# Performance work log

Measured on AMD Instinct MI355X. Metric: run time of the kernel, lower is better.

Reference implementation:

```python
import jax, jax.numpy as jnp
import numpy as np

B, T, V = 64, 8192, 50257


def setup_inputs() -> dict:
    key = jax.random.key(0)
    k1, k2, k3, k4 = jax.random.split(key, 4)
    ids = jax.random.randint(k1, (B, T), 1, V, dtype=jnp.int32)
    # give each row a random real length in [T//2, T], rest padding (pad_token_id=0)
    lens = jax.random.randint(k4, (B,), T // 2, T + 1, dtype=jnp.int32)
    pos = jnp.arange(T, dtype=jnp.int32)[None, :]
    input_ids = jnp.where(pos < lens[:, None], ids, 0)
    is_punct = jax.random.uniform(k2, (V,)) < 0.05
    is_abbreviation = jax.random.uniform(k3, (V,)) < 0.01
    return {
        "input_ids": input_ids,
        "is_punct": is_punct,
        "is_abbreviation": is_abbreviation,
        "max_phrase_len": 32,
        "pad_token_id": 0,
    }


def reference(input_ids, is_punct, is_abbreviation, max_phrase_len, pad_token_id):
    Bb, Tt = input_ids.shape
    # ---- compute_is_end ----
    punct_at_t = is_punct[input_ids]                               # (B,T)
    prev_ids = jnp.concatenate(
        [jnp.zeros((Bb, 1), input_ids.dtype), input_ids[:, :-1]], axis=1)
    prev_is_abbr = is_abbreviation[prev_ids].at[:, 0].set(False)
    is_real = input_ids != pad_token_id                            # (B,T)
    pos = jnp.arange(Tt, dtype=jnp.int32)
    pos_bt = jnp.broadcast_to(pos[None, :], (Bb, Tt))
    last_real = jnp.max(jnp.where(is_real, pos_bt, -1), axis=1)    # (B,)
    is_end0 = punct_at_t & ~prev_is_abbr & is_real                 # pre-scan boundaries

    def step(last_boundary, xs):
        e_t, t = xs
        forced = (t - last_boundary) >= max_phrase_len
        fire = (e_t | (last_real == t) | forced) & (t <= last_real)
        last_boundary = jnp.where(fire, t, last_boundary)
        return last_boundary, fire

    _, fires = jax.lax.scan(
        step, jnp.full((Bb,), -1, jnp.int32),
        (is_end0.T, jnp.arange(Tt, dtype=jnp.int32)))
    is_end = fires.T                                               # (B,T) bool

    # ---- pack_phrases_from_is_end (P padded to T upper bound) ----
    ie = is_end.astype(jnp.int32)
    phrase_id = jnp.concatenate(
        [jnp.zeros((Bb, 1), jnp.int32), jnp.cumsum(ie[:, :-1], axis=1)], axis=1)
    P = Tt
    rows = jnp.arange(Bb, dtype=jnp.int32)[:, None]
    first_pos = jnp.full((Bb, P), Tt, jnp.int32).at[rows, phrase_id].min(pos_bt)
    slot = pos_bt - jnp.take_along_axis(first_pos, phrase_id, axis=1)  # (B,T)
    in_range = (slot < max_phrase_len) & (slot >= 0) & is_real
    # route invalid entries to a dummy slot (index max_phrase_len), slice it off
    safe_slot = jnp.where(in_range, slot, max_phrase_len)
    mask_pad = jnp.zeros((Bb, P, max_phrase_len + 1), bool)
    mask_pad = mask_pad.at[rows, phrase_id, safe_slot].set(in_range)
    phrase_mask = mask_pad[:, :, :max_phrase_len]
    tok_pad = jnp.zeros((Bb, P, max_phrase_len + 1), jnp.int32)
    tok_pad = tok_pad.at[rows, phrase_id, safe_slot].set(jnp.where(in_range, pos_bt, 0))
    phrase_token_idx = tok_pad[:, :, :max_phrase_len]
    phrase_end_pos = jnp.full((Bb, P), -1, jnp.int32).at[rows, phrase_id].max(
        jnp.where(in_range, pos_bt, -1))
    return phrase_mask, phrase_token_idx, phrase_end_pos
```

## Files before the change

kernel.cpp:

```cpp
#include <hip/hip_runtime.h>
#include <stdint.h>

#define BB 64
#define TT 8192

#define WS_PAIR   4096

__device__ __forceinline__ unsigned long long bitsBelow(int e) {
    return (e >= 64) ? ~0ULL : ((1ULL << e) - 1ULL);
}

__device__ __forceinline__ bool lut(const void* tbl, int flag, int idx) {
    if (flag == 2) return ((const float*)tbl)[idx]   != 0.0f;
    if (flag == 1) return ((const uint8_t*)tbl)[idx] != 0;
    return ((const int*)tbl)[idx] != 0;
}

__global__ __launch_bounds__(256) void natural_kernel(
        const int* __restrict__ ids,
        const void* __restrict__ punct,
        const void* __restrict__ abbr,
        ulonglong2* __restrict__ pairW) {
    __shared__ int sFlag;
    if (threadIdx.x == 0) sFlag = 0;
    __syncthreads();
    {
        const uint32_t* w = (const uint32_t*)punct;
        bool byteGT1 = false, wordGT1 = false;
#pragma unroll
        for (int j = 0; j < 4; ++j) {
            uint32_t x = w[threadIdx.x * 4 + j];
            byteGT1 |= (x & 0xFEFEFEFEu) != 0u;
            wordGT1 |= (x > 1u);
        }
        int local = (byteGT1 ? 2 : 0) | (wordGT1 ? 1 : 0);
        if (local) atomicOr(&sFlag, local);
    }
    __syncthreads();
    int fl = sFlag;
    int flag = (fl & 2) ? 2 : (fl & 1);

    int g = blockIdx.x * 256 + threadIdx.x;
    int t = g & (TT - 1);
    int id = ids[g];
    bool real = (id != 0);
    bool isLR = real && ((t == TT - 1) || (ids[g + 1] == 0));
    bool e = false;
    if (real) {
        bool pu = lut(punct, flag, id);
        if (pu) {
            bool pa = (t > 0) ? lut(abbr, flag, ids[g - 1]) : false;
            e = !pa;
        }
    }
    bool natural = real && (e || isLR);
    unsigned long long nb = __ballot(natural);
    unsigned long long rb = __ballot(real);
    if ((threadIdx.x & 63) == 0) {
        pairW[g >> 6] = make_ulonglong2(nb, rb);
    }
}

__global__ __launch_bounds__(1024) void fill_kernel(
        const ulonglong2* __restrict__ pairW,
        int* __restrict__ out) {
    __shared__ int sFires[TT];
    __shared__ int sNf;

    int b     = blockIdx.x >> 3;
    int slice = blockIdx.x & 7;
    int tid   = threadIdx.x;
    int wave  = tid >> 6, lane = tid & 63;

    if (wave == 0) {
        ulonglong2 pA = pairW[b * 128 + lane];
        ulonglong2 pB = pairW[b * 128 + 64 + lane];
        unsigned long long nA = pA.x, rA = pA.y;
        unsigned long long nB = pB.x, rB = pB.y;
        int lnA = nA ? lane * 64 + 63 - __clzll(nA) : -1;
        int lnB = nB ? (lane + 64) * 64 + 63 - __clzll(nB) : -1;
        int sA = lnA;
        for (int d = 1; d < 64; d <<= 1) { int v = __shfl_up(sA, d); if (lane >= d) sA = max(sA, v); }
        int exA = __shfl_up(sA, 1); if (lane == 0) exA = -1;
        int totA = __shfl(sA, 63);
        int sB = lnB;
        for (int d = 1; d < 64; d <<= 1) { int v = __shfl_up(sB, d); if (lane >= d) sB = max(sB, v); }
        int exB = __shfl_up(sB, 1); if (lane == 0) exB = -1;
        exB = max(exB, totA);

        auto fireWord = [&](unsigned long long nw, unsigned long long rw,
                            int widx, int carry) -> unsigned long long {
            long long base = (long long)widx * 64;
            unsigned long long fire = 0, rem = nw;
            long long cur = carry;
            while (true) {
                int nxt = rem ? (__ffsll(rem) - 1) : 64;
                int r = (int)(((cur - base) % 32 + 32) % 32);
                unsigned long long pat = (1ULL << r) | (1ULL << (r + 32));
                int s = (int)(cur - base + 1); if (s < 0) s = 0;
                fire |= pat & bitsBelow(nxt) & ~bitsBelow(s);
                if (!rem) break;
                fire |= 1ULL << nxt;
                cur = base + nxt;
                rem &= rem - 1;
            }
            return fire & rw;
        };
        unsigned long long fA = fireWord(nA, rA, lane, exA);
        unsigned long long fB = fireWord(nB, rB, lane + 64, exB);
        int pcA = __popcll(fA), pcB = __popcll(fB);
        int iA = pcA;
        for (int d = 1; d < 64; d <<= 1) { int v = __shfl_up(iA, d); if (lane >= d) iA += v; }
        int baseA = iA - pcA;
        int totPA = __shfl(iA, 63);
        int iB = pcB;
        for (int d = 1; d < 64; d <<= 1) { int v = __shfl_up(iB, d); if (lane >= d) iB += v; }
        int baseB = totPA + iB - pcB;
        int total = totPA + __shfl(iB, 63);
        unsigned long long f = fA; int idx = baseA;
        while (f) { int t = __ffsll(f) - 1; sFires[idx++] = lane * 64 + t; f &= f - 1; }
        f = fB; idx = baseB;
        while (f) { int t = __ffsll(f) - 1; sFires[idx++] = (lane + 64) * 64 + t; f &= f - 1; }
        if (lane == 0) sNf = total;
    }
    __syncthreads();

    int nf = sNf;
    const long long MOFF = (long long)BB * TT * 32;
    int pbase = slice * 1024;
#pragma unroll
    for (int i = 0; i < 8; ++i) {
        int task = i * 1024 + tid;
        int q  = task & 7;
        int lp = task >> 3;
        int gp = pbase + lp;
        int4 mv, tv;
        if (gp < nf) {
            int end   = sFires[gp];
            int start = (gp > 0) ? (sFires[gp - 1] + 1) : 0;
            int len   = end - start + 1;
            int s0 = q * 4;
            int* mp = (int*)&mv;
            int* tp = (int*)&tv;
#pragma unroll
            for (int j = 0; j < 4; ++j) {
                int s = s0 + j;
                bool m = s < len;
                mp[j] = m ? 1 : 0;
                tp[j] = m ? (start + s) : 0;
            }
        } else {
            mv = make_int4(0, 0, 0, 0);
            tv = mv;
        }
        long long bp = (long long)b * TT + gp;
        *(int4*)(out + bp * 32 + q * 4)        = mv;
        *(int4*)(out + MOFF + bp * 32 + q * 4) = tv;
    }
    {
        int gp = pbase + tid;
        out[2 * MOFF + (long long)b * TT + gp] = (gp < nf) ? sFires[gp] : -1;
    }
}

extern "C" void kernel_launch(void* const* d_in, const int* in_sizes, int n_in,
                              void* d_out, int out_size, void* d_ws, size_t ws_size,
                              hipStream_t stream) {
    const int*  ids   = (const int*)d_in[0];
    const void* punct = d_in[1];
    const void* abbr  = d_in[2];
    char* ws = (char*)d_ws;
    ulonglong2* pairW = (ulonglong2*)(ws + WS_PAIR);
    int* out = (int*)d_out;

    natural_kernel<<<(BB * TT) / 256, 256, 0, stream>>>(ids, punct, abbr, pairW);
    fill_kernel   <<<BB * 8, 1024, 0, stream>>>(pairW, out);
}
```

Measured before the change: 32.06 us.

## Pack lookup tables into bitmaps and fuse boundary detection into fill kernel

A small first kernel now compresses the punctuation and abbreviation tables into bitmaps. The boundary-detection work moves into the fill kernel: each block reads its row's ids, looks them up in the bitmaps, and builds the natural and real bit words in shared memory. This removes the global pairW round trip, and the lookups hit a small, cache-friendly bitmap instead of the full table. The trade-off is that the row's ids are now read by all 8 slice blocks, and the lookup work is repeated 8 times per row.

Measured after the change: 37.09 us. +15.7%, slower.

```diff
diff --git a/kernel.cpp b/kernel.cpp
--- a/kernel.cpp
+++ b/kernel.cpp
@@ -3,8 +3,11 @@
 
 #define BB 64
 #define TT 8192
-
-#define WS_PAIR   4096
+#define VV 50257
+
+#define NBMW 1571
+#define WS_BMP   4096
+#define WS_BMA   (4096 + 6400)
 
 __device__ __forceinline__ unsigned long long bitsBelow(int e) {
     return (e >= 64) ? ~0ULL : ((1ULL << e) - 1ULL);
@@ -16,11 +19,9 @@
     return ((const int*)tbl)[idx] != 0;
 }
 
-__global__ __launch_bounds__(256) void natural_kernel(
-        const int* __restrict__ ids,
-        const void* __restrict__ punct,
-        const void* __restrict__ abbr,
-        ulonglong2* __restrict__ pairW) {
+__global__ __launch_bounds__(256) void bitmap_kernel(
+        const void* __restrict__ punct, const void* __restrict__ abbr,
+        uint32_t* __restrict__ bmP, uint32_t* __restrict__ bmA) {
     __shared__ int sFlag;
     if (threadIdx.x == 0) sFlag = 0;
     __syncthreads();
@@ -40,30 +41,26 @@
     int fl = sFlag;
     int flag = (fl & 2) ? 2 : (fl & 1);
 
-    int g = blockIdx.x * 256 + threadIdx.x;
-    int t = g & (TT - 1);
-    int id = ids[g];
-    bool real = (id != 0);
-    bool isLR = real && ((t == TT - 1) || (ids[g + 1] == 0));
-    bool e = false;
-    if (real) {
-        bool pu = lut(punct, flag, id);
-        if (pu) {
-            bool pa = (t > 0) ? lut(abbr, flag, ids[g - 1]) : false;
-            e = !pa;
-        }
-    }
-    bool natural = real && (e || isLR);
-    unsigned long long nb = __ballot(natural);
-    unsigned long long rb = __ballot(real);
+    int nb = (int)gridDim.x >> 1;
+    int isAbbr = blockIdx.x >= nb;
+    int j = isAbbr ? (blockIdx.x - nb) : blockIdx.x;
+    const void* tbl = isAbbr ? abbr : punct;
+    uint32_t* out   = isAbbr ? bmA : bmP;
+    int i = j * 256 + threadIdx.x;
+    bool bit = (i < VV) ? lut(tbl, flag, i) : false;
+    unsigned long long bal = __ballot(bit);
     if ((threadIdx.x & 63) == 0) {
-        pairW[g >> 6] = make_ulonglong2(nb, rb);
-    }
-}
-
-__global__ __launch_bounds__(1024) void fill_kernel(
-        const ulonglong2* __restrict__ pairW,
+        *(unsigned long long*)&out[i >> 5] = bal;
+    }
+}
+
+__global__ __launch_bounds__(1024) void mono_kernel(
+        const int* __restrict__ ids,
+        const uint32_t* __restrict__ bmP,
+        const uint32_t* __restrict__ bmA,
         int* __restrict__ out) {
+    __shared__ unsigned long long sNat[128], sReal[128];
+    __shared__ uint8_t sBN[1024], sBR[1024];
     __shared__ int sFires[TT];
     __shared__ int sNf;
 
@@ -72,11 +69,42 @@
     int tid   = threadIdx.x;
     int wave  = tid >> 6, lane = tid & 63;
 
+    const int* rowIds = ids + b * TT;
+    int base = tid * 8;
+    int4 va = *(const int4*)(rowIds + base);
+    int4 vc = *(const int4*)(rowIds + base + 4);
+    int id[9];
+    id[0]=va.x; id[1]=va.y; id[2]=va.z; id[3]=va.w;
+    id[4]=vc.x; id[5]=vc.y; id[6]=vc.z; id[7]=vc.w;
+    id[8] = (tid < 1023) ? rowIds[base + 8] : 0;
+    int prev = (tid > 0) ? rowIds[base - 1] : 0;
+    uint32_t nbits = 0, rbits = 0;
+#pragma unroll
+    for (int j = 0; j < 8; ++j) {
+        int idj = id[j];
+        bool real = (idj != 0);
+        bool isLR = real && ((base + j == TT - 1) || (id[j + 1] == 0));
+        bool e = false;
+        if (real && ((bmP[idj >> 5] >> (idj & 31)) & 1u)) {
+            int pid = j ? id[j - 1] : prev;
+            e = (base + j == 0) ? true : !((bmA[pid >> 5] >> (pid & 31)) & 1u);
+        }
+        bool nat = real && (e || isLR);
+        nbits |= (uint32_t)nat  << j;
+        rbits |= (uint32_t)real << j;
+    }
+    sBN[tid] = (uint8_t)nbits;
+    sBR[tid] = (uint8_t)rbits;
+    __syncthreads();
+    if (tid < 128) {
+        sNat[tid]  = *(const unsigned long long*)&sBN[tid * 8];
+        sReal[tid] = *(const unsigned long long*)&sBR[tid * 8];
+    }
+    __syncthreads();
+
     if (wave == 0) {
-        ulonglong2 pA = pairW[b * 128 + lane];
-        ulonglong2 pB = pairW[b * 128 + 64 + lane];
-        unsigned long long nA = pA.x, rA = pA.y;
-        unsigned long long nB = pB.x, rB = pB.y;
+        unsigned long long nA = sNat[lane],  nB = sNat[lane + 64];
+        unsigned long long rA = sReal[lane], rB = sReal[lane + 64];
         int lnA = nA ? lane * 64 + 63 - __clzll(nA) : -1;
         int lnB = nB ? (lane + 64) * 64 + 63 - __clzll(nB) : -1;
         int sA = lnA;
@@ -90,18 +118,18 @@
 
         auto fireWord = [&](unsigned long long nw, unsigned long long rw,
                             int widx, int carry) -> unsigned long long {
-            long long base = (long long)widx * 64;
+            long long wbase = (long long)widx * 64;
             unsigned long long fire = 0, rem = nw;
             long long cur = carry;
             while (true) {
                 int nxt = rem ? (__ffsll(rem) - 1) : 64;
-                int r = (int)(((cur - base) % 32 + 32) % 32);
+                int r = (int)(((cur - wbase) % 32 + 32) % 32);
                 unsigned long long pat = (1ULL << r) | (1ULL << (r + 32));
-                int s = (int)(cur - base + 1); if (s < 0) s = 0;
+                int s = (int)(cur - wbase + 1); if (s < 0) s = 0;
                 fire |= pat & bitsBelow(nxt) & ~bitsBelow(s);
                 if (!rem) break;
                 fire |= 1ULL << nxt;
-                cur = base + nxt;
+                cur = wbase + nxt;
                 rem &= rem - 1;
             }
             return fire & rw;
@@ -170,9 +198,11 @@
     const void* punct = d_in[1];
     const void* abbr  = d_in[2];
     char* ws = (char*)d_ws;
-    ulonglong2* pairW = (ulonglong2*)(ws + WS_PAIR);
+    uint32_t* bmP = (uint32_t*)(ws + WS_BMP);
+    uint32_t* bmA = (uint32_t*)(ws + WS_BMA);
     int* out = (int*)d_out;
 
-    natural_kernel<<<(BB * TT) / 256, 256, 0, stream>>>(ids, punct, abbr, pairW);
-    fill_kernel   <<<BB * 8, 1024, 0, stream>>>(pairW, out);
-}
+    const int nb = (VV + 255) / 256;
+    bitmap_kernel<<<2 * nb, 256, 0, stream>>>(punct, abbr, bmP, bmA);
+    mono_kernel  <<<BB * 8, 1024, 0, stream>>>(ids, bmP, bmA, out);
+}
```

## Zero outputs in first kernel and write only active phrases per row

Applied to the files above, without the earlier changes.

The background zero/-1 fill of the mask, token-index and end-position outputs moves into the first, highly parallel ballot kernel, so it no longer waits behind the serial per-row fire scan. The second kernel now runs one block per row instead of eight, which removes the redundant repetition of the wave-0 scan, and it writes only the populated phrases. In exchange, the entries of active phrases are written twice (once as zeros, then with values), and the second kernel launches only 64 blocks.

After: 31.29 us. -2.4%, faster.

```diff
diff --git a/kernel.cpp b/kernel.cpp
--- a/kernel.cpp
+++ b/kernel.cpp
@@ -5,6 +5,8 @@
 #define TT 8192
 
 #define WS_PAIR   4096
+
+#define MOFF ((long long)BB * TT * 32)
 
 __device__ __forceinline__ unsigned long long bitsBelow(int e) {
     return (e >= 64) ? ~0ULL : ((1ULL << e) - 1ULL);
@@ -16,11 +18,12 @@
     return ((const int*)tbl)[idx] != 0;
 }
 
-__global__ __launch_bounds__(256) void natural_kernel(
+__global__ __launch_bounds__(256) void bg_kernel(
         const int* __restrict__ ids,
         const void* __restrict__ punct,
         const void* __restrict__ abbr,
-        ulonglong2* __restrict__ pairW) {
+        ulonglong2* __restrict__ pairW,
+        int* __restrict__ out) {
     __shared__ int sFlag;
     if (threadIdx.x == 0) sFlag = 0;
     __syncthreads();
@@ -39,6 +42,16 @@
     __syncthreads();
     int fl = sFlag;
     int flag = (fl & 2) ? 2 : (fl & 1);
+
+    {
+        long long zbase = (long long)blockIdx.x * 16384;
+        int4 z = make_int4(0, 0, 0, 0);
+#pragma unroll
+        for (int k = 0; k < 16; ++k) {
+            *(int4*)(out + zbase + k * 1024 + threadIdx.x * 4) = z;
+        }
+        out[2 * MOFF + blockIdx.x * 256 + threadIdx.x] = -1;
+    }
 
     int g = blockIdx.x * 256 + threadIdx.x;
     int t = g & (TT - 1);
@@ -61,16 +74,15 @@
     }
 }
 
-__global__ __launch_bounds__(1024) void fill_kernel(
+__global__ __launch_bounds__(1024) void sparse_kernel(
         const ulonglong2* __restrict__ pairW,
         int* __restrict__ out) {
     __shared__ int sFires[TT];
     __shared__ int sNf;
 
-    int b     = blockIdx.x >> 3;
-    int slice = blockIdx.x & 7;
-    int tid   = threadIdx.x;
-    int wave  = tid >> 6, lane = tid & 63;
+    int b    = blockIdx.x;
+    int tid  = threadIdx.x;
+    int wave = tid >> 6, lane = tid & 63;
 
     if (wave == 0) {
         ulonglong2 pA = pairW[b * 128 + lane];
@@ -90,18 +102,18 @@
 
         auto fireWord = [&](unsigned long long nw, unsigned long long rw,
                             int widx, int carry) -> unsigned long long {
-            long long base = (long long)widx * 64;
+            long long wbase = (long long)widx * 64;
             unsigned long long fire = 0, rem = nw;
             long long cur = carry;
             while (true) {
                 int nxt = rem ? (__ffsll(rem) - 1) : 64;
-                int r = (int)(((cur - base) % 32 + 32) % 32);
+                int r = (int)(((cur - wbase) % 32 + 32) % 32);
                 unsigned long long pat = (1ULL << r) | (1ULL << (r + 32));
-                int s = (int)(cur - base + 1); if (s < 0) s = 0;
+                int s = (int)(cur - wbase + 1); if (s < 0) s = 0;
                 fire |= pat & bitsBelow(nxt) & ~bitsBelow(s);
                 if (!rem) break;
                 fire |= 1ULL << nxt;
-                cur = base + nxt;
+                cur = wbase + nxt;
                 rem &= rem - 1;
             }
             return fire & rw;
@@ -126,40 +138,28 @@
     __syncthreads();
 
     int nf = sNf;
-    const long long MOFF = (long long)BB * TT * 32;
-    int pbase = slice * 1024;
+    int ntask = nf * 8;
+    for (int task = tid; task < ntask; task += 1024) {
+        int q = task & 7;
+        int p = task >> 3;
+        int end   = sFires[p];
+        int start = (p > 0) ? (sFires[p - 1] + 1) : 0;
+        int len   = end - start + 1;
+        int s0 = q * 4;
+        int4 mv, tv;
+        int* mp = (int*)&mv;
+        int* tp = (int*)&tv;
 #pragma unroll
-    for (int i = 0; i < 8; ++i) {
-        int task = i * 1024 + tid;
-        int q  = task & 7;
-        int lp = task >> 3;
-        int gp = pbase + lp;
-        int4 mv, tv;
-        if (gp < nf) {
-            int end   = sFires[gp];
-            int start = (gp > 0) ? (sFires[gp - 1] + 1) : 0;
-            int len   = end - start + 1;
-            int s0 = q * 4;
-            int* mp = (int*)&mv;
-            int* tp = (int*)&tv;
-#pragma unroll
-            for (int j = 0; j < 4; ++j) {
-                int s = s0 + j;
-                bool m = s < len;
-                mp[j] = m ? 1 : 0;
-                tp[j] = m ? (start + s) : 0;
-            }
-        } else {
-            mv = make_int4(0, 0, 0, 0);
-            tv = mv;
+        for (int j = 0; j < 4; ++j) {
+            int s = s0 + j;
+            bool m = s < len;
+            mp[j] = m ? 1 : 0;
+            tp[j] = m ? (start + s) : 0;
         }
-        long long bp = (long long)b * TT + gp;
+        long long bp = (long long)b * TT + p;
         *(int4*)(out + bp * 32 + q * 4)        = mv;
         *(int4*)(out + MOFF + bp * 32 + q * 4) = tv;
-    }
-    {
-        int gp = pbase + tid;
-        out[2 * MOFF + (long long)b * TT + gp] = (gp < nf) ? sFires[gp] : -1;
+        if (q == 0) out[2 * MOFF + bp] = end;
     }
 }
 
@@ -173,6 +173,6 @@
     ulonglong2* pairW = (ulonglong2*)(ws + WS_PAIR);
     int* out = (int*)d_out;
 
-    natural_kernel<<<(BB * TT) / 256, 256, 0, stream>>>(ids, punct, abbr, pairW);
-    fill_kernel   <<<BB * 8, 1024, 0, stream>>>(pairW, out);
+    bg_kernel    <<<(BB * TT) / 256, 256, 0, stream>>>(ids, punct, abbr, pairW, out);
+    sparse_kernel<<<BB, 1024, 0, stream>>>(pairW, out);
 }
```
